# Kernel tuning notes

Hardware: AMD Instinct MI355X
Metric: run time of the kernel (lower is better)

## Reference

```python
import jax, jax.numpy as jnp
import numpy as np
from jax import lax

N_QUBITS = 8
N_LAYERS = 7


def _conv(x, w, b, stride, pad):
    y = lax.conv_general_dilated(x, w, (stride, stride), [(pad, pad), (pad, pad)],
                                 dimension_numbers=('NCHW', 'OIHW', 'NCHW'))
    return y + b[None, :, None, None]


def _apply_1q(psi, M, q):
    # psi: (B, 2,2,...,2); apply 2x2 real matrix M on qubit q (axis q+1)
    a = q + 1
    pm = jnp.moveaxis(psi, a, 1)
    out = jnp.einsum('ij,bj...->bi...', M, pm)
    return jnp.moveaxis(out, 1, a)


def _apply_cnot(psi, c, t):
    ac, at = c + 1, t + 1
    pm = jnp.moveaxis(psi, (ac, at), (1, 2))
    top = pm[:, 0]
    bot = jnp.flip(pm[:, 1], axis=1)  # flip target when control=1
    pm = jnp.stack([top, bot], axis=1)
    return jnp.moveaxis(pm, (1, 2), (ac, at))


def _quantum(features, qw):
    psi = features / jnp.linalg.norm(features, axis=1, keepdims=True)
    B = psi.shape[0]
    psi = psi.reshape((B,) + (2,) * N_QUBITS)
    for l in range(N_LAYERS):
        for q in range(N_QUBITS):
            th = qw[l, q] / 2.0
            c, s = jnp.cos(th), jnp.sin(th)
            M = jnp.stack([jnp.stack([c, -s]), jnp.stack([s, c])])
            psi = _apply_1q(psi, M, q)
        for q in range(N_QUBITS - 1):
            psi = _apply_cnot(psi, q, q + 1)
    p = psi.reshape(B, 2, -1) ** 2
    return jnp.sum(p[:, 0], axis=1) - jnp.sum(p[:, 1], axis=1)  # <PauliZ(0)>


def setup_inputs() -> dict:
    key = jax.random.key(0)
    ks = jax.random.split(key, 20)
    def g(k, shape, fan_in):
        return jax.random.normal(k, shape, jnp.float32) * (1.0 / np.sqrt(fan_in))
    inp = {
        'x':  jax.random.normal(ks[0], (4096, 1, 64, 64), jnp.float32),
        'w1': g(ks[1], (4, 1, 5, 5), 25), 'b1': jnp.zeros((4,), jnp.float32),
        'w2': g(ks[2], (8, 4, 3, 3), 36), 'b2': jnp.zeros((8,), jnp.float32),
        'w3': g(ks[3], (16, 8, 3, 3), 72), 'b3': jnp.zeros((16,), jnp.float32),
        'wf': g(ks[4], (256, 64), 64), 'bf': jnp.zeros((256,), jnp.float32),
        'qw': jax.random.uniform(ks[5], (7, 8), jnp.float32, 0.0, 2 * np.pi),
        'wc1': g(ks[6], (200, 1), 1),   'bc1': jnp.zeros((200,), jnp.float32),
        'wc2': g(ks[7], (150, 200), 200), 'bc2': jnp.zeros((150,), jnp.float32),
        'wc3': g(ks[8], (100, 150), 150), 'bc3': jnp.zeros((100,), jnp.float32),
        'wc4': g(ks[9], (50, 100), 100),  'bc4': jnp.zeros((50,), jnp.float32),
        'wc5': g(ks[10], (1, 50), 50),    'bc5': jnp.zeros((1,), jnp.float32),
    }
    return inp


def reference(x, w1, b1, w2, b2, w3, b3, wf, bf, qw,
              wc1, bc1, wc2, bc2, wc3, bc3, wc4, bc4, wc5, bc5):
    # CNN feature extractor (dropout = identity at inference)
    h = jax.nn.relu(_conv(x, w1, b1, 2, 2))   # (B,4,32,32)
    h = jax.nn.relu(_conv(h, w2, b2, 2, 1))   # (B,8,16,16)
    h = jax.nn.relu(_conv(h, w3, b3, 1, 1))   # (B,16,16,16)
    B = h.shape[0]
    # AdaptiveAvgPool2d(2): 16x16 -> 2x2 via 8x8 non-overlapping means
    h = h.reshape(B, 16, 2, 8, 2, 8).mean(axis=(3, 5))  # (B,16,2,2)
    h = h.reshape(B, 64)
    feats = jax.nn.relu(h @ wf.T + bf)        # (B,256)
    # F.normalize(p=2, dim=1)
    feats = feats / jnp.maximum(jnp.linalg.norm(feats, axis=1, keepdims=True), 1e-12)
    # Batched 8-qubit statevector simulation (replaces per-sample Python loop)
    q = _quantum(feats, qw)[:, None]          # (B,1)
    # MLP classifier
    h = jax.nn.relu(q @ wc1.T + bc1)
    h = jax.nn.relu(h @ wc2.T + bc2)
    h = jax.nn.relu(h @ wc3.T + bc3)
    h = jax.nn.relu(h @ wc4.T + bc4)
    return jax.nn.sigmoid(h @ wc5.T + bc5)    # (B,1)
```

## Files before the change

### kernel.cpp

```cpp
#include <hip/hip_runtime.h>
#include <math.h>

__global__ __launch_bounds__(256, 6)
void convpool_kernel(const float* __restrict__ x,
                     const float* __restrict__ w1, const float* __restrict__ b1,
                     const float* __restrict__ w2, const float* __restrict__ b2,
                     const float* __restrict__ w3, const float* __restrict__ b3,
                     float* __restrict__ poolout)
{
    __shared__ __align__(16) float arena[4620];
    __shared__ __align__(16) float w3s[1168];
    const int tid  = threadIdx.x;
    const int b    = blockIdx.x;
    const int lane = tid & 63;

    for (int i = tid; i < 1168; i += 256) w3s[i] = (i < 1152) ? w3[i] : b3[i - 1152];
    for (int i = tid; i < 140; i += 256) { int oc = i / 35, c = i - oc * 35; arena[oc * 1155 + c] = 0.f; }
    for (int i = tid; i < 132; i += 256) { int oc = i / 33, r = i - oc * 33; arena[oc * 1155 + r * 35] = 0.f; }

    {
        const float* xb = x + (size_t)b * 4096;
        const int oh  = tid >> 3;
        const int ow  = tid & 7;
        const int ow0 = ow * 4;
        const int c0  = ow0 * 2 - 2;
        const bool cmL = (ow == 0);
        const bool cmR = (ow == 7);
        float acc[4][4];
        #pragma unroll
        for (int oc = 0; oc < 4; oc++) {
            const float bv = b1[oc];
            #pragma unroll
            for (int j = 0; j < 4; j++) acc[oc][j] = bv;
        }
        #pragma unroll
        for (int kh = 0; kh < 5; kh++) {
            const int ih = oh * 2 - 2 + kh;
            if (ih >= 0 && ih < 64) {
                const float* row = xb + ih * 64;
                float colv[11];
                {
                    float v0 = row[cmL ? 0 : c0];
                    float v1 = row[cmL ? 0 : c0 + 1];
                    float vA = row[cmR ? 63 : c0 + 10];
                    colv[0]  = cmL ? 0.f : v0;
                    colv[1]  = cmL ? 0.f : v1;
                    colv[10] = cmR ? 0.f : vA;
                }
                #pragma unroll
                for (int cc = 2; cc < 10; cc++) colv[cc] = row[c0 + cc];
                #pragma unroll
                for (int kw = 0; kw < 5; kw++) {
                    #pragma unroll
                    for (int oc = 0; oc < 4; oc++) {
                        const float wv = w1[oc * 25 + kh * 5 + kw];
                        acc[oc][0] = fmaf(colv[0 + kw], wv, acc[oc][0]);
                        acc[oc][1] = fmaf(colv[2 + kw], wv, acc[oc][1]);
                        acc[oc][2] = fmaf(colv[4 + kw], wv, acc[oc][2]);
                        acc[oc][3] = fmaf(colv[6 + kw], wv, acc[oc][3]);
                    }
                }
            }
        }
        #pragma unroll
        for (int oc = 0; oc < 4; oc++) {
            float* o = arena + oc * 1155 + (oh + 1) * 35 + ow0 + 1;
            #pragma unroll
            for (int j = 0; j < 4; j++) o[j] = fmaxf(acc[oc][j], 0.f);
        }
    }
    __syncthreads();

    float r2[2][4];
    {
        const int oc0 = __builtin_amdgcn_readfirstlane(tid >> 6);
        const int oh  = lane >> 2, ow0 = (lane & 3) * 4;
        {
            const float ba = b2[oc0], bb = b2[oc0 + 4];
            #pragma unroll
            for (int j = 0; j < 4; j++) { r2[0][j] = ba; r2[1][j] = bb; }
        }
        const int c0s = ow0 * 2;
        #pragma unroll
        for (int ic = 0; ic < 4; ic++) {
            const float* base = arena + ic * 1155;
            #pragma unroll
            for (int kh = 0; kh < 3; kh++) {
                const int ihs = oh * 2 + kh;
                float colv[9];
                #pragma unroll
                for (int cc = 0; cc < 9; cc++) colv[cc] = base[ihs * 35 + c0s + cc];
                #pragma unroll
                for (int kw = 0; kw < 3; kw++) {
                    const float wa = w2[((oc0    ) * 4 + ic) * 9 + kh * 3 + kw];
                    const float wb = w2[((oc0 + 4) * 4 + ic) * 9 + kh * 3 + kw];
                    #pragma unroll
                    for (int j = 0; j < 4; j++) {
                        r2[0][j] = fmaf(colv[2 * j + kw], wa, r2[0][j]);
                        r2[1][j] = fmaf(colv[2 * j + kw], wb, r2[1][j]);
                    }
                }
            }
        }
    }
    __syncthreads();

    for (int i = tid; i < 576; i += 256) {
        const int ch = i / 72, j = i - ch * 72;
        if (j < 18)      arena[ch * 324 + j] = 0.f;
        else if (j < 36) arena[ch * 324 + 17 * 18 + (j - 18)] = 0.f;
        else if (j < 52) arena[ch * 324 + (j - 35) * 18] = 0.f;
        else if (j < 68) arena[ch * 324 + (j - 51) * 18 + 17] = 0.f;
    }
    {
        const int oc0 = __builtin_amdgcn_readfirstlane(tid >> 6);
        const int oh  = lane >> 2, ow0 = (lane & 3) * 4;
        float* oA = arena + oc0 * 324       + (oh + 1) * 18 + ow0 + 1;
        float* oB = arena + (oc0 + 4) * 324 + (oh + 1) * 18 + ow0 + 1;
        #pragma unroll
        for (int j = 0; j < 4; j++) { oA[j] = fmaxf(r2[0][j], 0.f); oB[j] = fmaxf(r2[1][j], 0.f); }
    }
    __syncthreads();

    {
        const int oc = tid >> 4, s = tid & 15;
        const int tr = (s >> 2) * 4, tc = (s & 3) * 4;
        float acc[16];
        const float bv = w3s[1152 + oc];
        #pragma unroll
        for (int k = 0; k < 16; k++) acc[k] = bv;
        #pragma unroll
        for (int ic = 0; ic < 8; ic++) {
            const float* xc = arena + ic * 324;
            float p[6][6];
            #pragma unroll
            for (int dr = 0; dr < 6; dr++)
                #pragma unroll
                for (int dc = 0; dc < 6; dc++)
                    p[dr][dc] = xc[(tr + dr) * 18 + (tc + dc)];
            float wv[9];
            #pragma unroll
            for (int k = 0; k < 9; k++) wv[k] = w3s[oc * 72 + ic * 9 + k];
            #pragma unroll
            for (int r = 0; r < 4; r++)
                #pragma unroll
                for (int c = 0; c < 4; c++) {
                    float a = acc[r * 4 + c];
                    #pragma unroll
                    for (int kh = 0; kh < 3; kh++)
                        #pragma unroll
                        for (int kw = 0; kw < 3; kw++)
                            a = fmaf(p[r + kh][c + kw], wv[kh * 3 + kw], a);
                    acc[r * 4 + c] = a;
                }
        }
        float ps = 0.f;
        #pragma unroll
        for (int k = 0; k < 16; k++) ps += fmaxf(acc[k], 0.f);
        ps += __shfl_xor(ps, 1, 64);
        ps += __shfl_xor(ps, 4, 64);
        if ((s & 5) == 0) {
            const int ii = s >> 3, jj = (s >> 1) & 1;
            poolout[b * 64 + oc * 4 + ii * 2 + jj] = ps * (1.f / 64.f);
        }
    }
}

__global__ __launch_bounds__(256)
void head_kernel(const float* __restrict__ poolin,
                 const float* __restrict__ wf, const float* __restrict__ bf,
                 const float* __restrict__ qw,
                 const float* __restrict__ wc1, const float* __restrict__ bc1,
                 const float* __restrict__ wc2, const float* __restrict__ bc2,
                 const float* __restrict__ wc3, const float* __restrict__ bc3,
                 const float* __restrict__ wc4, const float* __restrict__ bc4,
                 const float* __restrict__ wc5, const float* __restrict__ bc5,
                 float* __restrict__ out)
{
    __shared__ __align__(16) float pool_s[256];
    __shared__ __align__(16) float feats[1024];
    __shared__ __align__(16) float h1[800];
    __shared__ __align__(16) float h2[600];
    __shared__ __align__(16) float h3[400];
    __shared__ __align__(16) float h4[200];
    __shared__ float zbuf[4];
    __shared__ float csc[56], css[56];

    const int tid  = threadIdx.x;
    const int blk  = blockIdx.x;
    const int lane = tid & 63;
    const int wv   = tid >> 6;

    pool_s[tid] = poolin[(size_t)blk * 256 + tid];
    if (tid < 56) {
        float th = qw[tid] * 0.5f;
        csc[tid] = cosf(th);
        css[tid] = sinf(th);
    }
    __syncthreads();

    {
        float acc[4];
        const float bv = bf[tid];
        #pragma unroll
        for (int e = 0; e < 4; e++) acc[e] = bv;
        const float4* wr = (const float4*)(wf + tid * 64);
        #pragma unroll
        for (int kc = 0; kc < 4; kc++) {
            float4 w0 = wr[kc * 4 + 0], w1_ = wr[kc * 4 + 1], w2_ = wr[kc * 4 + 2], w3_ = wr[kc * 4 + 3];
            #pragma unroll
            for (int e = 0; e < 4; e++) {
                const float4* pp = (const float4*)(pool_s + e * 64 + kc * 16);
                float4 p0 = pp[0], p1 = pp[1], p2 = pp[2], p3 = pp[3];
                float a = acc[e];
                a = fmaf(w0.x, p0.x, a); a = fmaf(w0.y, p0.y, a); a = fmaf(w0.z, p0.z, a); a = fmaf(w0.w, p0.w, a);
                a = fmaf(w1_.x, p1.x, a); a = fmaf(w1_.y, p1.y, a); a = fmaf(w1_.z, p1.z, a); a = fmaf(w1_.w, p1.w, a);
                a = fmaf(w2_.x, p2.x, a); a = fmaf(w2_.y, p2.y, a); a = fmaf(w2_.z, p2.z, a); a = fmaf(w2_.w, p2.w, a);
                a = fmaf(w3_.x, p3.x, a); a = fmaf(w3_.y, p3.y, a); a = fmaf(w3_.z, p3.z, a); a = fmaf(w3_.w, p3.w, a);
                acc[e] = a;
            }
        }
        #pragma unroll
        for (int e = 0; e < 4; e++) feats[e * 256 + tid] = fmaxf(acc[e], 0.f);
    }
    __syncthreads();

    {
        const float* base = feats + wv * 256;
        float v0 = base[lane], v1 = base[64 + lane];
        float v2 = base[128 + lane], v3 = base[192 + lane];
        float ssq = v0 * v0 + v1 * v1 + v2 * v2 + v3 * v3;
        #pragma unroll
        for (int off = 1; off < 64; off <<= 1) ssq += __shfl_xor(ssq, off, 64);
        const float inv = 1.0f / fmaxf(sqrtf(ssq), 1e-12f);
        v0 *= inv; v1 *= inv; v2 *= inv; v3 *= inv;

        for (int l = 0; l < 7; l++) {
            {
                float c = csc[l * 8 + 0], s = css[l * 8 + 0];
                float n0 = c * v0 - s * v2, n2 = s * v0 + c * v2;
                float n1 = c * v1 - s * v3, n3 = s * v1 + c * v3;
                float c1 = csc[l * 8 + 1], s1 = css[l * 8 + 1];
                v0 = c1 * n0 - s1 * n1; v1 = s1 * n0 + c1 * n1;
                v2 = c1 * n2 - s1 * n3; v3 = s1 * n2 + c1 * n3;
            }
            #pragma unroll
            for (int q = 2; q < 8; q++) {
                const int m = 1 << (7 - q);
                const float c = csc[l * 8 + q], s = css[l * 8 + q];
                const float sgn = (lane & m) ? s : -s;
                float t0 = __shfl_xor(v0, m, 64);
                float t1 = __shfl_xor(v1, m, 64);
                float t2 = __shfl_xor(v2, m, 64);
                float t3 = __shfl_xor(v3, m, 64);
                v0 = fmaf(sgn, t0, c * v0);
                v1 = fmaf(sgn, t1, c * v1);
                v2 = fmaf(sgn, t2, c * v2);
                v3 = fmaf(sgn, t3, c * v3);
            }
            { float t = v2; v2 = v3; v3 = t; }
            v1 = __shfl_xor(v1, 32, 64);
            v3 = __shfl_xor(v3, 32, 64);
            #pragma unroll
            for (int q = 2; q < 7; q++) {
                const int mc = 1 << (7 - q), mt = 1 << (6 - q);
                float t0 = __shfl_xor(v0, mt, 64);
                float t1 = __shfl_xor(v1, mt, 64);
                float t2 = __shfl_xor(v2, mt, 64);
                float t3 = __shfl_xor(v3, mt, 64);
                if (lane & mc) { v0 = t0; v1 = t1; v2 = t2; v3 = t3; }
            }
        }
        float m0 = v0 * v0 + v1 * v1 - v2 * v2 - v3 * v3;
        #pragma unroll
        for (int off = 1; off < 64; off <<= 1) m0 += __shfl_xor(m0, off, 64);
        if (lane == 0) zbuf[wv] = m0;
    }
    __syncthreads();

    if (tid < 200) {
        const float w = wc1[tid], bv = bc1[tid];
        #pragma unroll
        for (int e = 0; e < 4; e++) h1[e * 200 + tid] = fmaxf(fmaf(zbuf[e], w, bv), 0.f);
    }
    __syncthreads();
    if (tid < 150) {
        float acc[4];
        const float bv = bc2[tid];
        #pragma unroll
        for (int e = 0; e < 4; e++) acc[e] = bv;
        const float4* wr = (const float4*)(wc2 + tid * 200);
        for (int kc = 0; kc < 25; kc++) {
            float4 wa = wr[2 * kc], wb = wr[2 * kc + 1];
            #pragma unroll
            for (int e = 0; e < 4; e++) {
                const float4* hp = (const float4*)(h1 + e * 200) + 2 * kc;
                float4 ha = hp[0], hb = hp[1];
                float a = acc[e];
                a = fmaf(wa.x, ha.x, a); a = fmaf(wa.y, ha.y, a); a = fmaf(wa.z, ha.z, a); a = fmaf(wa.w, ha.w, a);
                a = fmaf(wb.x, hb.x, a); a = fmaf(wb.y, hb.y, a); a = fmaf(wb.z, hb.z, a); a = fmaf(wb.w, hb.w, a);
                acc[e] = a;
            }
        }
        #pragma unroll
        for (int e = 0; e < 4; e++) h2[e * 150 + tid] = fmaxf(acc[e], 0.f);
    }
    __syncthreads();
    if (tid < 100) {
        float acc[4];
        const float bv = bc3[tid];
        #pragma unroll
        for (int e = 0; e < 4; e++) acc[e] = bv;
        const float2* wr = (const float2*)(wc3 + tid * 150);
        for (int k = 0; k < 75; k++) {
            float2 wa = wr[k];
            #pragma unroll
            for (int e = 0; e < 4; e++) {
                float2 hv = ((const float2*)(h2 + e * 150))[k];
                acc[e] = fmaf(wa.x, hv.x, fmaf(wa.y, hv.y, acc[e]));
            }
        }
        #pragma unroll
        for (int e = 0; e < 4; e++) h3[e * 100 + tid] = fmaxf(acc[e], 0.f);
    }
    __syncthreads();
    if (tid < 50) {
        float acc[4];
        const float bv = bc4[tid];
        #pragma unroll
        for (int e = 0; e < 4; e++) acc[e] = bv;
        const float4* wr = (const float4*)(wc4 + tid * 100);
        for (int kc = 0; kc < 25; kc++) {
            float4 wa = wr[kc];
            #pragma unroll
            for (int e = 0; e < 4; e++) {
                float4 hv = ((const float4*)(h3 + e * 100))[kc];
                float a = acc[e];
                a = fmaf(wa.x, hv.x, a); a = fmaf(wa.y, hv.y, a);
                a = fmaf(wa.z, hv.z, a); a = fmaf(wa.w, hv.w, a);
                acc[e] = a;
            }
        }
        #pragma unroll
        for (int e = 0; e < 4; e++) h4[e * 50 + tid] = fmaxf(acc[e], 0.f);
    }
    __syncthreads();
    if (tid < 4) {
        float acc = bc5[0];
        const float2* wr = (const float2*)wc5;
        #pragma unroll
        for (int k = 0; k < 25; k++) {
            float2 wa = wr[k];
            float2 hv = ((const float2*)(h4 + tid * 50))[k];
            acc = fmaf(wa.x, hv.x, fmaf(wa.y, hv.y, acc));
        }
        out[blk * 4 + tid] = 1.0f / (1.0f + expf(-acc));
    }
}

extern "C" void kernel_launch(void* const* d_in, const int* in_sizes, int n_in,
                              void* d_out, int out_size, void* d_ws, size_t ws_size,
                              hipStream_t stream) {
    const float* x   = (const float*)d_in[0];
    const float* w1  = (const float*)d_in[1];
    const float* b1  = (const float*)d_in[2];
    const float* w2  = (const float*)d_in[3];
    const float* b2  = (const float*)d_in[4];
    const float* w3  = (const float*)d_in[5];
    const float* b3  = (const float*)d_in[6];
    const float* wf  = (const float*)d_in[7];
    const float* bf  = (const float*)d_in[8];
    const float* qw  = (const float*)d_in[9];
    const float* wc1 = (const float*)d_in[10];
    const float* bc1 = (const float*)d_in[11];
    const float* wc2 = (const float*)d_in[12];
    const float* bc2 = (const float*)d_in[13];
    const float* wc3 = (const float*)d_in[14];
    const float* bc3 = (const float*)d_in[15];
    const float* wc4 = (const float*)d_in[16];
    const float* bc4 = (const float*)d_in[17];
    const float* wc5 = (const float*)d_in[18];
    const float* bc5 = (const float*)d_in[19];
    float* out = (float*)d_out;

    float* poolbuf = (float*)d_ws;

    convpool_kernel<<<4096, 256, 0, stream>>>(x, w1, b1, w2, b2, w3, b3, poolbuf);
    head_kernel<<<1024, 256, 0, stream>>>(poolbuf, wf, bf, qw,
                                          wc1, bc1, wc2, bc2, wc3, bc3,
                                          wc4, bc4, wc5, bc5, out);
}
```

Measured before the change: 218.5 us.

## Fuse conv/pool and head into one kernel, one sample per block

Merges the conv-pool kernel and the head kernel into a single kernel where each block processes one sample end to end. The FC layer, quantum simulation and MLP now run from shared memory reused out of the conv arena. This removes the second launch and the global round-trip of pooled features. In exchange, the head's weight loads are no longer amortised over 4 samples per block, and most threads sit idle in the serial MLP tail of every block, so each weight is re-read 4096 times.

After: 263.4 us. 20.6% more time.

```diff
diff --git a/kernel.cpp b/kernel.cpp
--- a/kernel.cpp
+++ b/kernel.cpp
@@ -2,19 +2,40 @@
 #include <math.h>
 
 __global__ __launch_bounds__(256, 6)
-void convpool_kernel(const float* __restrict__ x,
-                     const float* __restrict__ w1, const float* __restrict__ b1,
-                     const float* __restrict__ w2, const float* __restrict__ b2,
-                     const float* __restrict__ w3, const float* __restrict__ b3,
-                     float* __restrict__ poolout)
+void fused_all(const float* __restrict__ x,
+               const float* __restrict__ w1, const float* __restrict__ b1,
+               const float* __restrict__ w2, const float* __restrict__ b2,
+               const float* __restrict__ w3, const float* __restrict__ b3,
+               const float* __restrict__ wf, const float* __restrict__ bf,
+               const float* __restrict__ qw,
+               const float* __restrict__ wc1, const float* __restrict__ bc1,
+               const float* __restrict__ wc2, const float* __restrict__ bc2,
+               const float* __restrict__ wc3, const float* __restrict__ bc3,
+               const float* __restrict__ wc4, const float* __restrict__ bc4,
+               const float* __restrict__ wc5, const float* __restrict__ bc5,
+               float* __restrict__ out)
 {
     __shared__ __align__(16) float arena[4620];
     __shared__ __align__(16) float w3s[1168];
+    __shared__ __align__(16) float csang[113];
+
+    float* pool  = arena;
+    float* feats = arena + 64;
+    float* h1    = arena + 320;
+    float* h2    = arena + 520;
+    float* h3    = arena + 672;
+    float* h4    = arena + 772;
+
     const int tid  = threadIdx.x;
     const int b    = blockIdx.x;
     const int lane = tid & 63;
 
     for (int i = tid; i < 1168; i += 256) w3s[i] = (i < 1152) ? w3[i] : b3[i - 1152];
+    if (tid < 56) {
+        float th = qw[tid] * 0.5f;
+        csang[tid]      = cosf(th);
+        csang[56 + tid] = sinf(th);
+    }
     for (int i = tid; i < 140; i += 256) { int oc = i / 35, c = i - oc * 35; arena[oc * 1155 + c] = 0.f; }
     for (int i = tid; i < 132; i += 256) { int oc = i / 33, r = i - oc * 33; arena[oc * 1155 + r * 35] = 0.f; }
 
@@ -122,6 +143,8 @@
     }
     __syncthreads();
 
+    float ps;
+    int psw;
     {
         const int oc = tid >> 4, s = tid & 15;
         const int tr = (s >> 2) * 4, tc = (s & 3) * 4;
@@ -154,81 +177,38 @@
                     acc[r * 4 + c] = a;
                 }
         }
-        float ps = 0.f;
+        ps = 0.f;
         #pragma unroll
         for (int k = 0; k < 16; k++) ps += fmaxf(acc[k], 0.f);
         ps += __shfl_xor(ps, 1, 64);
         ps += __shfl_xor(ps, 4, 64);
-        if ((s & 5) == 0) {
-            const int ii = s >> 3, jj = (s >> 1) & 1;
-            poolout[b * 64 + oc * 4 + ii * 2 + jj] = ps * (1.f / 64.f);
-        }
-    }
-}
-
-__global__ __launch_bounds__(256)
-void head_kernel(const float* __restrict__ poolin,
-                 const float* __restrict__ wf, const float* __restrict__ bf,
-                 const float* __restrict__ qw,
-                 const float* __restrict__ wc1, const float* __restrict__ bc1,
-                 const float* __restrict__ wc2, const float* __restrict__ bc2,
-                 const float* __restrict__ wc3, const float* __restrict__ bc3,
-                 const float* __restrict__ wc4, const float* __restrict__ bc4,
-                 const float* __restrict__ wc5, const float* __restrict__ bc5,
-                 float* __restrict__ out)
-{
-    __shared__ __align__(16) float pool_s[256];
-    __shared__ __align__(16) float feats[1024];
-    __shared__ __align__(16) float h1[800];
-    __shared__ __align__(16) float h2[600];
-    __shared__ __align__(16) float h3[400];
-    __shared__ __align__(16) float h4[200];
-    __shared__ float zbuf[4];
-    __shared__ float csc[56], css[56];
-
-    const int tid  = threadIdx.x;
-    const int blk  = blockIdx.x;
-    const int lane = tid & 63;
-    const int wv   = tid >> 6;
-
-    pool_s[tid] = poolin[(size_t)blk * 256 + tid];
-    if (tid < 56) {
-        float th = qw[tid] * 0.5f;
-        csc[tid] = cosf(th);
-        css[tid] = sinf(th);
-    }
-    __syncthreads();
-
-    {
-        float acc[4];
-        const float bv = bf[tid];
-        #pragma unroll
-        for (int e = 0; e < 4; e++) acc[e] = bv;
+        const int ii = s >> 3, jj = (s >> 1) & 1;
+        psw = ((s & 5) == 0) ? (oc * 4 + ii * 2 + jj) : -1;
+    }
+    __syncthreads();
+    if (psw >= 0) pool[psw] = ps * (1.f / 64.f);
+    __syncthreads();
+
+    {
+        float acc = bf[tid];
         const float4* wr = (const float4*)(wf + tid * 64);
+        const float4* pl = (const float4*)pool;
         #pragma unroll
         for (int kc = 0; kc < 4; kc++) {
             float4 w0 = wr[kc * 4 + 0], w1_ = wr[kc * 4 + 1], w2_ = wr[kc * 4 + 2], w3_ = wr[kc * 4 + 3];
-            #pragma unroll
-            for (int e = 0; e < 4; e++) {
-                const float4* pp = (const float4*)(pool_s + e * 64 + kc * 16);
-                float4 p0 = pp[0], p1 = pp[1], p2 = pp[2], p3 = pp[3];
-                float a = acc[e];
-                a = fmaf(w0.x, p0.x, a); a = fmaf(w0.y, p0.y, a); a = fmaf(w0.z, p0.z, a); a = fmaf(w0.w, p0.w, a);
-                a = fmaf(w1_.x, p1.x, a); a = fmaf(w1_.y, p1.y, a); a = fmaf(w1_.z, p1.z, a); a = fmaf(w1_.w, p1.w, a);
-                a = fmaf(w2_.x, p2.x, a); a = fmaf(w2_.y, p2.y, a); a = fmaf(w2_.z, p2.z, a); a = fmaf(w2_.w, p2.w, a);
-                a = fmaf(w3_.x, p3.x, a); a = fmaf(w3_.y, p3.y, a); a = fmaf(w3_.z, p3.z, a); a = fmaf(w3_.w, p3.w, a);
-                acc[e] = a;
-            }
-        }
-        #pragma unroll
-        for (int e = 0; e < 4; e++) feats[e * 256 + tid] = fmaxf(acc[e], 0.f);
-    }
-    __syncthreads();
-
-    {
-        const float* base = feats + wv * 256;
-        float v0 = base[lane], v1 = base[64 + lane];
-        float v2 = base[128 + lane], v3 = base[192 + lane];
+            float4 p0 = pl[kc * 4 + 0], p1 = pl[kc * 4 + 1], p2 = pl[kc * 4 + 2], p3 = pl[kc * 4 + 3];
+            acc = fmaf(w0.x, p0.x, acc); acc = fmaf(w0.y, p0.y, acc); acc = fmaf(w0.z, p0.z, acc); acc = fmaf(w0.w, p0.w, acc);
+            acc = fmaf(w1_.x, p1.x, acc); acc = fmaf(w1_.y, p1.y, acc); acc = fmaf(w1_.z, p1.z, acc); acc = fmaf(w1_.w, p1.w, acc);
+            acc = fmaf(w2_.x, p2.x, acc); acc = fmaf(w2_.y, p2.y, acc); acc = fmaf(w2_.z, p2.z, acc); acc = fmaf(w2_.w, p2.w, acc);
+            acc = fmaf(w3_.x, p3.x, acc); acc = fmaf(w3_.y, p3.y, acc); acc = fmaf(w3_.z, p3.z, acc); acc = fmaf(w3_.w, p3.w, acc);
+        }
+        feats[tid] = fmaxf(acc, 0.f);
+    }
+    __syncthreads();
+
+    if (tid < 64) {
+        float v0 = feats[lane], v1 = feats[64 + lane];
+        float v2 = feats[128 + lane], v3 = feats[192 + lane];
         float ssq = v0 * v0 + v1 * v1 + v2 * v2 + v3 * v3;
         #pragma unroll
         for (int off = 1; off < 64; off <<= 1) ssq += __shfl_xor(ssq, off, 64);
@@ -237,17 +217,17 @@
 
         for (int l = 0; l < 7; l++) {
             {
-                float c = csc[l * 8 + 0], s = css[l * 8 + 0];
+                float c = csang[l * 8 + 0], s = csang[56 + l * 8 + 0];
                 float n0 = c * v0 - s * v2, n2 = s * v0 + c * v2;
                 float n1 = c * v1 - s * v3, n3 = s * v1 + c * v3;
-                float c1 = csc[l * 8 + 1], s1 = css[l * 8 + 1];
+                float c1 = csang[l * 8 + 1], s1 = csang[56 + l * 8 + 1];
                 v0 = c1 * n0 - s1 * n1; v1 = s1 * n0 + c1 * n1;
                 v2 = c1 * n2 - s1 * n3; v3 = s1 * n2 + c1 * n3;
             }
             #pragma unroll
             for (int q = 2; q < 8; q++) {
                 const int m = 1 << (7 - q);
-                const float c = csc[l * 8 + q], s = css[l * 8 + q];
+                const float c = csang[l * 8 + q], s = csang[56 + l * 8 + q];
                 const float sgn = (lane & m) ? s : -s;
                 float t0 = __shfl_xor(v0, m, 64);
                 float t1 = __shfl_xor(v1, m, 64);
@@ -274,87 +254,62 @@
         float m0 = v0 * v0 + v1 * v1 - v2 * v2 - v3 * v3;
         #pragma unroll
         for (int off = 1; off < 64; off <<= 1) m0 += __shfl_xor(m0, off, 64);
-        if (lane == 0) zbuf[wv] = m0;
-    }
-    __syncthreads();
-
-    if (tid < 200) {
-        const float w = wc1[tid], bv = bc1[tid];
-        #pragma unroll
-        for (int e = 0; e < 4; e++) h1[e * 200 + tid] = fmaxf(fmaf(zbuf[e], w, bv), 0.f);
-    }
+        if (lane == 0) csang[112] = m0;
+    }
+    __syncthreads();
+
+    const float z = csang[112];
+    if (tid < 200) h1[tid] = fmaxf(fmaf(z, wc1[tid], bc1[tid]), 0.f);
     __syncthreads();
     if (tid < 150) {
-        float acc[4];
-        const float bv = bc2[tid];
-        #pragma unroll
-        for (int e = 0; e < 4; e++) acc[e] = bv;
+        float acc = bc2[tid];
         const float4* wr = (const float4*)(wc2 + tid * 200);
+        const float4* hp = (const float4*)h1;
+        #pragma unroll 5
         for (int kc = 0; kc < 25; kc++) {
             float4 wa = wr[2 * kc], wb = wr[2 * kc + 1];
-            #pragma unroll
-            for (int e = 0; e < 4; e++) {
-                const float4* hp = (const float4*)(h1 + e * 200) + 2 * kc;
-                float4 ha = hp[0], hb = hp[1];
-                float a = acc[e];
-                a = fmaf(wa.x, ha.x, a); a = fmaf(wa.y, ha.y, a); a = fmaf(wa.z, ha.z, a); a = fmaf(wa.w, ha.w, a);
-                a = fmaf(wb.x, hb.x, a); a = fmaf(wb.y, hb.y, a); a = fmaf(wb.z, hb.z, a); a = fmaf(wb.w, hb.w, a);
-                acc[e] = a;
-            }
-        }
-        #pragma unroll
-        for (int e = 0; e < 4; e++) h2[e * 150 + tid] = fmaxf(acc[e], 0.f);
+            float4 ha = hp[2 * kc], hb = hp[2 * kc + 1];
+            acc = fmaf(wa.x, ha.x, acc); acc = fmaf(wa.y, ha.y, acc); acc = fmaf(wa.z, ha.z, acc); acc = fmaf(wa.w, ha.w, acc);
+            acc = fmaf(wb.x, hb.x, acc); acc = fmaf(wb.y, hb.y, acc); acc = fmaf(wb.z, hb.z, acc); acc = fmaf(wb.w, hb.w, acc);
+        }
+        h2[tid] = fmaxf(acc, 0.f);
     }
     __syncthreads();
     if (tid < 100) {
-        float acc[4];
-        const float bv = bc3[tid];
-        #pragma unroll
-        for (int e = 0; e < 4; e++) acc[e] = bv;
+        float acc = bc3[tid];
         const float2* wr = (const float2*)(wc3 + tid * 150);
+        const float2* hp = (const float2*)h2;
+        #pragma unroll 15
         for (int k = 0; k < 75; k++) {
-            float2 wa = wr[k];
-            #pragma unroll
-            for (int e = 0; e < 4; e++) {
-                float2 hv = ((const float2*)(h2 + e * 150))[k];
-                acc[e] = fmaf(wa.x, hv.x, fmaf(wa.y, hv.y, acc[e]));
-            }
-        }
-        #pragma unroll
-        for (int e = 0; e < 4; e++) h3[e * 100 + tid] = fmaxf(acc[e], 0.f);
+            float2 wa = wr[k], hv = hp[k];
+            acc = fmaf(wa.x, hv.x, fmaf(wa.y, hv.y, acc));
+        }
+        h3[tid] = fmaxf(acc, 0.f);
     }
     __syncthreads();
     if (tid < 50) {
-        float acc[4];
-        const float bv = bc4[tid];
-        #pragma unroll
-        for (int e = 0; e < 4; e++) acc[e] = bv;
+        float acc = bc4[tid];
         const float4* wr = (const float4*)(wc4 + tid * 100);
+        const float4* hp = (const float4*)h3;
+        #pragma unroll
         for (int kc = 0; kc < 25; kc++) {
-            float4 wa = wr[kc];
-            #pragma unroll
-            for (int e = 0; e < 4; e++) {
-                float4 hv = ((const float4*)(h3 + e * 100))[kc];
-                float a = acc[e];
-                a = fmaf(wa.x, hv.x, a); a = fmaf(wa.y, hv.y, a);
-                a = fmaf(wa.z, hv.z, a); a = fmaf(wa.w, hv.w, a);
-                acc[e] = a;
-            }
-        }
-        #pragma unroll
-        for (int e = 0; e < 4; e++) h4[e * 50 + tid] = fmaxf(acc[e], 0.f);
-    }
-    __syncthreads();
-    if (tid < 4) {
+            float4 wa = wr[kc], hv = hp[kc];
+            acc = fmaf(wa.x, hv.x, acc); acc = fmaf(wa.y, hv.y, acc);
+            acc = fmaf(wa.z, hv.z, acc); acc = fmaf(wa.w, hv.w, acc);
+        }
+        h4[tid] = fmaxf(acc, 0.f);
+    }
+    __syncthreads();
+    if (tid == 0) {
         float acc = bc5[0];
         const float2* wr = (const float2*)wc5;
+        const float2* hp = (const float2*)h4;
         #pragma unroll
         for (int k = 0; k < 25; k++) {
-            float2 wa = wr[k];
-            float2 hv = ((const float2*)(h4 + tid * 50))[k];
+            float2 wa = wr[k], hv = hp[k];
             acc = fmaf(wa.x, hv.x, fmaf(wa.y, hv.y, acc));
         }
-        out[blk * 4 + tid] = 1.0f / (1.0f + expf(-acc));
+        out[b] = 1.0f / (1.0f + expf(-acc));
     }
 }
 
@@ -383,10 +338,7 @@
     const float* bc5 = (const float*)d_in[19];
     float* out = (float*)d_out;
 
-    float* poolbuf = (float*)d_ws;
-
-    convpool_kernel<<<4096, 256, 0, stream>>>(x, w1, b1, w2, b2, w3, b3, poolbuf);
-    head_kernel<<<1024, 256, 0, stream>>>(poolbuf, wf, bf, qw,
-                                          wc1, bc1, wc2, bc2, wc3, bc3,
-                                          wc4, bc4, wc5, bc5, out);
+    fused_all<<<4096, 256, 0, stream>>>(x, w1, b1, w2, b2, w3, b3, wf, bf, qw,
+                                        wc1, bc1, wc2, bc2, wc3, bc3,
+                                        wc4, bc4, wc5, bc5, out);
 }
```
